# Optimization experiments

Measured on AMD Instinct MI355X. Metric: run time of the kernel, lower is better.

Reference implementation:

```python
import jax, jax.numpy as jnp
import numpy as np

D_MODEL = 5120
NUM_HEADS = 128
HEAD_DIM = D_MODEL // NUM_HEADS  # 40
LATENT = 1536


def setup_inputs() -> dict:
    key = jax.random.key(0)
    ks = jax.random.split(key, 9)
    B, S = 2, 1024
    scale = 0.02
    return {
        "x": jax.random.normal(ks[0], (B, S, D_MODEL), dtype=jnp.float32),
        "Wq": jax.random.normal(ks[1], (D_MODEL, D_MODEL), dtype=jnp.float32) * scale,
        "bq": jnp.zeros((D_MODEL,), dtype=jnp.float32),
        "Wc": jax.random.normal(ks[2], (D_MODEL, LATENT), dtype=jnp.float32) * scale,
        "bc": jnp.zeros((LATENT,), dtype=jnp.float32),
        "Wk": jax.random.normal(ks[3], (LATENT, D_MODEL), dtype=jnp.float32) * scale,
        "bk": jnp.zeros((D_MODEL,), dtype=jnp.float32),
        "Wv": jax.random.normal(ks[4], (LATENT, D_MODEL), dtype=jnp.float32) * scale,
        "bv": jnp.zeros((D_MODEL,), dtype=jnp.float32),
    }


def reference(x, Wq, bq, Wc, bc, Wk, bk, Wv, bv):
    B, S, _ = x.shape
    H, Dh = NUM_HEADS, HEAD_DIM
    # projections
    q = x @ Wq + bq                     # [B,S,D]
    kv_latent = x @ Wc + bc             # [B,S,L]
    k = kv_latent @ Wk + bk             # [B,S,D]
    v = kv_latent @ Wv + bv             # [B,S,D]
    # split heads -> [B,H,S,Dh]
    q = q.reshape(B, S, H, Dh).transpose(0, 2, 1, 3)
    k = k.reshape(B, S, H, Dh).transpose(0, 2, 1, 3)
    v = v.reshape(B, S, H, Dh).transpose(0, 2, 1, 3)
    scores = jnp.einsum("bhqd,bhkd->bhqk", q, k) / jnp.sqrt(jnp.float32(Dh))
    attn = jax.nn.softmax(scores, axis=-1)
    out = jnp.einsum("bhqk,bhkd->bhqd", attn, v)  # [B,H,S,Dh]
    return out.transpose(0, 2, 1, 3).reshape(B, S, H * Dh)
```

## Files before the change

kernel.cpp:

```cpp
#include <hip/hip_runtime.h>
#include <hip/hip_bf16.h>

typedef __attribute__((ext_vector_type(8))) __bf16 bf16x8;
typedef __attribute__((ext_vector_type(4))) __bf16 bf16x4;
typedef __attribute__((ext_vector_type(4))) float f32x4;

#define MFMA16(a, b, c) __builtin_amdgcn_mfma_f32_16x16x32_bf16((a), (b), (c), 0, 0, 0)

#if __has_builtin(__builtin_amdgcn_exp2f)
#define EXP2F(x) __builtin_amdgcn_exp2f(x)
#else
#define EXP2F(x) exp2f(x)
#endif

#define GLDS16(g, l)                                                             \
    __builtin_amdgcn_global_load_lds((const __attribute__((address_space(1))) void*)(g), \
                                     (__attribute__((address_space(3))) void*)(l), 16, 0, 0)

#define BARRIER()                          \
    do {                                   \
        asm volatile("" ::: "memory");     \
        __builtin_amdgcn_s_barrier();      \
        asm volatile("" ::: "memory");     \
    } while (0)

#define WAIT_LGKM0() asm volatile("s_waitcnt lgkmcnt(0)" ::: "memory")
#define VM6 asm volatile("s_waitcnt vmcnt(6)" ::: "memory")
#define VM8 asm volatile("s_waitcnt vmcnt(8)" ::: "memory")
#define VM0 asm volatile("s_waitcnt vmcnt(0)" ::: "memory")
#define VMNONE ((void)0)
#define KEEP(x) x
#define DROP(x)

static __device__ __forceinline__ unsigned short cvt_bf(float f) {
    return __builtin_bit_cast(unsigned short, (__bf16)f);
}

static __device__ __forceinline__ bf16x8 bf8_zero() {
    uint4 z = make_uint4(0, 0, 0, 0);
    return __builtin_bit_cast(bf16x8, z);
}

__global__ __launch_bounds__(256) void xconv(const float* __restrict__ X,
                                             unsigned short* __restrict__ Xb, int n) {
    int i = (blockIdx.x * 256 + threadIdx.x) * 4;
    if (i < n) {
        float4 f = *(const float4*)(X + i);
        ushort4 o;
        o.x = cvt_bf(f.x); o.y = cvt_bf(f.y); o.z = cvt_bf(f.z); o.w = cvt_bf(f.w);
        *(ushort4*)(Xb + i) = o;
    }
}

__global__ __launch_bounds__(256) void wconv(const float* __restrict__ W,
                                             unsigned short* __restrict__ WT, int K, int N) {
    __shared__ unsigned short tile[32][33];
    int n0 = blockIdx.x * 32, k0 = blockIdx.y * 32;
    int c = threadIdx.x & 31, r8 = threadIdx.x >> 5;
#pragma unroll
    for (int it = 0; it < 4; ++it) {
        int r = r8 + it * 8;
        tile[r][c] = cvt_bf(W[(size_t)(k0 + r) * N + n0 + c]);
    }
    __syncthreads();
    int k2 = (threadIdx.x & 15) * 2, n8 = threadIdx.x >> 4;
#pragma unroll
    for (int it = 0; it < 2; ++it) {
        int n = n8 + it * 16;
        ushort2 o;
        o.x = tile[k2][n];
        o.y = tile[k2 + 1][n];
        *(ushort2*)&WT[(size_t)(n0 + n) * K + k0 + k2] = o;
    }
}

#define STAGE_A(S, H, KT)                                                              \
    do {                                                                               \
        GLDS16(aS[H][0] + (size_t)(KT) * 64, &Abuf[S][(H) * 8192 + wid * 512]);        \
        GLDS16(aS[H][1] + (size_t)(KT) * 64, &Abuf[S][(H) * 8192 + 4096 + wid * 512]); \
    } while (0)
#define STAGE_B(S, H, KT)                                                              \
    do {                                                                               \
        GLDS16(bS[H][0] + (size_t)(KT) * 64, &Bbuf[S][(H) * 8192 + wid * 512]);        \
        GLDS16(bS[H][1] + (size_t)(KT) * 64, &Bbuf[S][(H) * 8192 + 4096 + wid * 512]); \
    } while (0)

#define LDA_HALF(S, QM)                                                                   \
    do {                                                                                  \
        _Pragma("unroll") for (int mi = 0; mi < 4; ++mi)                                  \
            _Pragma("unroll") for (int kh = 0; kh < 2; ++kh)                              \
                af[mi][kh] =                                                              \
                    *(const bf16x8*)&Abuf[S][((QM) * 8192 + aoff + mi * 1024) ^ (kh * 32)]; \
    } while (0)
#define LDB_HALF(S, QN, BF)                                                               \
    do {                                                                                  \
        _Pragma("unroll") for (int ni = 0; ni < 2; ++ni)                                  \
            _Pragma("unroll") for (int kh = 0; kh < 2; ++kh)                              \
                BF[ni][kh] =                                                              \
                    *(const bf16x8*)&Bbuf[S][((QN) * 8192 + boff + ni * 1024) ^ (kh * 32)]; \
    } while (0)

#define MMAQ(QM, QN, BF)                                                                \
    do {                                                                                \
        _Pragma("unroll") for (int mi = 0; mi < 4; ++mi)                                \
            _Pragma("unroll") for (int ni = 0; ni < 2; ++ni)                            \
                _Pragma("unroll") for (int kh = 0; kh < 2; ++kh)                        \
                    acc[(QM) * 4 + mi][(QN) * 2 + ni] =                                 \
                        MFMA16(af[mi][kh], BF[ni][kh], acc[(QM) * 4 + mi][(QN) * 2 + ni]); \
    } while (0)

#define KTILE(S, T, STG1, STG234, VMOP)             \
    {                                               \
        const int s_ = (S);                         \
        LDA_HALF(s_, 0);                            \
        LDB_HALF(s_, 0, bf0);                       \
        STG1(STAGE_B(s_ ^ 1, 0, (T) + 1);)          \
        asm volatile("s_waitcnt lgkmcnt(8)" ::: "memory"); \
        BARRIER();                                  \
        WAIT_LGKM0();                               \
        __builtin_amdgcn_s_setprio(1);              \
        MMAQ(0, 0, bf0);                            \
        __builtin_amdgcn_s_setprio(0);              \
        BARRIER();                                  \
        LDB_HALF(s_, 1, bf1);                       \
        STG234(STAGE_A(s_, 0, (T) + 2);)            \
        BARRIER();                                  \
        WAIT_LGKM0();                               \
        __builtin_amdgcn_s_setprio(1);              \
        MMAQ(0, 1, bf1);                            \
        __builtin_amdgcn_s_setprio(0);              \
        BARRIER();                                  \
        LDA_HALF(s_, 1);                            \
        STG234(STAGE_B(s_, 1, (T) + 2);)            \
        BARRIER();                                  \
        WAIT_LGKM0();                               \
        __builtin_amdgcn_s_setprio(1);              \
        MMAQ(1, 1, bf1);                            \
        __builtin_amdgcn_s_setprio(0);              \
        BARRIER();                                  \
        STG234(STAGE_A(s_, 1, (T) + 2);)            \
        VMOP;                                       \
        BARRIER();                                  \
        __builtin_amdgcn_s_setprio(1);              \
        MMAQ(1, 0, bf0);                            \
        __builtin_amdgcn_s_setprio(0);              \
        BARRIER();                                  \
    }

__global__ __launch_bounds__(512, 2) void gemm256(const unsigned short* __restrict__ A, int lda,
                                                  const unsigned short* __restrict__ BT, int ldb,
                                                  const float* __restrict__ bias0,
                                                  const float* __restrict__ bias1, int nsplit,
                                                  unsigned short* __restrict__ C, int ldc,
                                                  int K, float s0, float s1, int gx) {
    __shared__ __align__(16) unsigned short Abuf[2][16384];
    __shared__ __align__(16) unsigned short Bbuf[2][16384];

    int nwg = gridDim.x, orig = blockIdx.x;
    int cpx = nwg >> 3;
    int wgid = (orig & 7) * cpx + (orig >> 3);
    int tm = wgid / gx, tn = wgid % gx;
    int m0 = tm * 256, n0 = tn * 256;

    int tid = threadIdx.x, lane = tid & 63, wid = tid >> 6;
    int wm = wid >> 2, wn = wid & 3;
    int lrow = lane & 15, lkg = lane >> 4;

    int t5 = tid >> 3;
    int cole = ((tid & 7) ^ ((tid >> 3) & 7)) << 3;
    const unsigned short* aS[2][2];
    const unsigned short* bS[2][2];
#pragma unroll
    for (int H = 0; H < 2; ++H)
#pragma unroll
        for (int c = 0; c < 2; ++c) {
            int rA = (c << 7) | (H << 6) | t5;
            int rB = (((c << 1) | (t5 >> 5)) << 6) | (H << 5) | (t5 & 31);
            aS[H][c] = A + (size_t)(m0 + rA) * lda + cole;
            bS[H][c] = BT + (size_t)(n0 + rB) * ldb + cole;
        }

    int xorc = (lkg * 8) ^ ((lrow & 7) << 3);
    int aoff = wm * 4096 + lrow * 64 + xorc;
    int boff = wn * 2048 + lrow * 64 + xorc;

    f32x4 acc[8][4];
#pragma unroll
    for (int i = 0; i < 8; ++i)
#pragma unroll
        for (int j = 0; j < 4; ++j) acc[i][j] = (f32x4){0.f, 0.f, 0.f, 0.f};
    bf16x8 af[4][2], bf0[2][2], bf1[2][2];

    const int nkt = K >> 6;

    STAGE_A(0, 0, 0); STAGE_A(0, 1, 0); STAGE_B(0, 0, 0); STAGE_B(0, 1, 0);
    STAGE_A(1, 0, 1); STAGE_B(1, 1, 1); STAGE_A(1, 1, 1);
    VM6;
    BARRIER();

    int t = 0;
    for (; t + 2 < nkt; ++t) KTILE(t & 1, t, KEEP, KEEP, VM6);
    KTILE(t & 1, t, KEEP, DROP, VM0);
    ++t;
    KTILE(t & 1, t, DROP, DROP, VMNONE);

#pragma unroll
    for (int ni = 0; ni < 4; ++ni) {
        int col = n0 + wn * 64 + ni * 16 + lrow;
        float bval = (col < nsplit) ? bias0[col] : bias1[col - nsplit];
        float scl = (col < nsplit) ? s0 : s1;
#pragma unroll
        for (int mi = 0; mi < 8; ++mi) {
            int row = m0 + wm * 128 + mi * 16 + lkg * 4;
#pragma unroll
            for (int j = 0; j < 4; ++j)
                C[(size_t)(row + j) * ldc + col] = cvt_bf((acc[mi][ni][j] + bval) * scl);
        }
    }
}

#define STG128(S, KT)                                                                  \
    do {                                                                               \
        _Pragma("unroll") for (int i_ = 0; i_ < 4; ++i_)                               \
            GLDS16(Ag + (size_t)(i_ * 32) * lda + (size_t)(KT) * 64,                   \
                   &Abuf[S][i_ * 2048 + wid * 512]);                                   \
        _Pragma("unroll") for (int i_ = 0; i_ < 4; ++i_)                               \
            GLDS16(Bg + (size_t)(i_ * 32) * ldb + (size_t)(KT) * 64,                   \
                   &Bbuf[S][i_ * 2048 + wid * 512]);                                   \
    } while (0)

__global__ __launch_bounds__(256, 2) void gemm128(const unsigned short* __restrict__ A, int lda,
                                                  const unsigned short* __restrict__ BT, int ldb,
                                                  const float* __restrict__ bias0,
                                                  const float* __restrict__ bias1, int nsplit,
                                                  unsigned short* __restrict__ C, int ldc,
                                                  int K, float s0, float s1, int gy) {
    __shared__ __align__(16) unsigned short Abuf[2][8192];
    __shared__ __align__(16) unsigned short Bbuf[2][8192];

    int b = blockIdx.x;
    int tm = b % gy, tn = b / gy;
    int m0 = tm * 128, n0 = tn * 128;
    int tid = threadIdx.x, lane = tid & 63, wid = tid >> 6;
    int wm = wid >> 1, wn = wid & 1;
    int lrow = lane & 15, lkg = lane >> 4;

    int srow = tid >> 3;
    int cole = ((tid & 7) ^ ((tid >> 3) & 7)) << 3;
    const unsigned short* Ag = A + (size_t)(m0 + srow) * lda + cole;
    const unsigned short* Bg = BT + (size_t)(n0 + srow) * ldb + cole;

    int xorc8 = (lrow & 7) << 3;
    int aoff = (wm * 64 + lrow) * 64;
    int boff = (wn * 64 + lrow) * 64;

    f32x4 acc[4][4];
#pragma unroll
    for (int i = 0; i < 4; ++i)
#pragma unroll
        for (int j = 0; j < 4; ++j) acc[i][j] = (f32x4){0.f, 0.f, 0.f, 0.f};

    const int nkt = K >> 6;
    STG128(0, 0);
    for (int t = 0; t < nkt; ++t) {
        const int cur = t & 1;
        if (t + 1 < nkt) {
            STG128(cur ^ 1, t + 1);
            VM8;
        } else {
            VM0;
        }
        BARRIER();
        bf16x8 af[4][2], bv[4][2];
#pragma unroll
        for (int mi = 0; mi < 4; ++mi)
#pragma unroll
            for (int kh = 0; kh < 2; ++kh)
                af[mi][kh] = *(const bf16x8*)&Abuf[cur][aoff + mi * 1024 + (((kh * 4 + lkg) << 3) ^ xorc8)];
#pragma unroll
        for (int ni = 0; ni < 4; ++ni)
#pragma unroll
            for (int kh = 0; kh < 2; ++kh)
                bv[ni][kh] = *(const bf16x8*)&Bbuf[cur][boff + ni * 1024 + (((kh * 4 + lkg) << 3) ^ xorc8)];
        __builtin_amdgcn_s_setprio(1);
#pragma unroll
        for (int mi = 0; mi < 4; ++mi)
#pragma unroll
            for (int ni = 0; ni < 4; ++ni)
#pragma unroll
                for (int kh = 0; kh < 2; ++kh)
                    acc[mi][ni] = MFMA16(af[mi][kh], bv[ni][kh], acc[mi][ni]);
        __builtin_amdgcn_s_setprio(0);
        BARRIER();
    }

#pragma unroll
    for (int ni = 0; ni < 4; ++ni) {
        int col = n0 + wn * 64 + ni * 16 + lrow;
        float bval = (col < nsplit) ? bias0[col] : bias1[col - nsplit];
        float scl = (col < nsplit) ? s0 : s1;
#pragma unroll
        for (int mi = 0; mi < 4; ++mi) {
            int row = m0 + wm * 64 + mi * 16 + lkg * 4;
#pragma unroll
            for (int j = 0; j < 4; ++j)
                C[(size_t)(row + j) * ldc + col] = cvt_bf((acc[mi][ni][j] + bval) * scl);
        }
    }
}

__global__ __launch_bounds__(256) void attn(const unsigned short* __restrict__ q, int ldq,
                                            const unsigned short* __restrict__ k, int ldk,
                                            const unsigned short* __restrict__ v, int ldv,
                                            float* __restrict__ out) {
    const int S = 1024, D = 5120, Dh = 40;
    int b = blockIdx.z, h = blockIdx.y, qt = blockIdx.x;
    int t = threadIdx.x, lane = t & 63, wid = t >> 6;
    int lrow = lane & 15, lkg = lane >> 4;

    __shared__ __align__(16) unsigned short Ks[64 * 72];
    __shared__ __align__(16) unsigned short Vs[64 * 72];
    __shared__ __align__(16) unsigned short Ps[4][16 * 72];

    const size_t qbase = ((size_t)b * S) * ldq + (size_t)h * Dh;
    const size_t kbase = ((size_t)b * S) * ldk + (size_t)h * Dh;
    const size_t vbase = ((size_t)b * S) * ldv + (size_t)h * Dh;
    int q0 = qt * 64 + wid * 16;

    bf16x8 qf0, qf1;
    {
        const unsigned short* qp = q + qbase + (size_t)(q0 + lrow) * ldq;
        qf0 = *(const bf16x8*)(qp + lkg * 8);
        qf1 = (lkg == 0) ? *(const bf16x8*)(qp + 32) : bf8_zero();
    }

    f32x4 acc[3];
#pragma unroll
    for (int nb = 0; nb < 3; ++nb) acc[nb] = (f32x4){0.f, 0.f, 0.f, 0.f};
    float mrun = -INFINITY, lrun = 0.f;

    for (int kt = 0; kt < 16; ++kt) {
        __syncthreads();
#pragma unroll
        for (int it = 0; it < 2; ++it) {
            int idx = t + it * 256;
            int rr = idx >> 3, cc = idx & 7;
            uint4 val = make_uint4(0, 0, 0, 0);
            if (cc < 5) val = *(const uint4*)(k + kbase + (size_t)(kt * 64 + rr) * ldk + cc * 8);
            *(uint4*)&Ks[rr * 72 + cc * 8] = val;
        }
#pragma unroll
        for (int it = 0; it < 2; ++it) {
            int idx = t + it * 256;
            int rr = idx & 63, cc = idx >> 6;
            if (cc < 6) {
                uint4 val = make_uint4(0, 0, 0, 0);
                if (cc < 5) val = *(const uint4*)(v + vbase + (size_t)(kt * 64 + rr) * ldv + cc * 8);
                const unsigned short* pv = (const unsigned short*)&val;
#pragma unroll
                for (int j = 0; j < 8; ++j) Vs[(cc * 8 + j) * 72 + rr] = pv[j];
            }
        }
        __syncthreads();

        f32x4 sf[4];
#pragma unroll
        for (int nb = 0; nb < 4; ++nb) {
            sf[nb] = (f32x4){0.f, 0.f, 0.f, 0.f};
            bf16x8 kf0 = *(const bf16x8*)&Ks[(nb * 16 + lrow) * 72 + lkg * 8];
            bf16x8 kf1 = *(const bf16x8*)&Ks[(nb * 16 + lrow) * 72 + 32 + lkg * 8];
            sf[nb] = MFMA16(kf0, qf0, sf[nb]);
            sf[nb] = MFMA16(kf1, qf1, sf[nb]);
        }

        float tm = sf[0][0];
#pragma unroll
        for (int nb = 0; nb < 4; ++nb)
#pragma unroll
            for (int i = 0; i < 4; ++i) tm = fmaxf(tm, sf[nb][i]);
        tm = fmaxf(tm, __shfl_xor(tm, 16));
        tm = fmaxf(tm, __shfl_xor(tm, 32));
        float mn = fmaxf(mrun, tm);
        float al = EXP2F(mrun - mn);
        mrun = mn;
        float rs = 0.f;
#pragma unroll
        for (int nb = 0; nb < 4; ++nb) {
            bf16x4 pk;
#pragma unroll
            for (int i = 0; i < 4; ++i) {
                float p = EXP2F(sf[nb][i] - mn);
                rs += p;
                pk[i] = (__bf16)p;
            }
            *(bf16x4*)&Ps[wid][lrow * 72 + nb * 16 + lkg * 4] = pk;
        }
        rs += __shfl_xor(rs, 16);
        rs += __shfl_xor(rs, 32);
        lrun = lrun * al + rs;

        float alr[4];
#pragma unroll
        for (int i = 0; i < 4; ++i) alr[i] = __shfl(al, lkg * 4 + i);
#pragma unroll
        for (int nb = 0; nb < 3; ++nb)
#pragma unroll
            for (int i = 0; i < 4; ++i) acc[nb][i] *= alr[i];

#pragma unroll
        for (int kk = 0; kk < 2; ++kk) {
            bf16x8 pf = *(const bf16x8*)&Ps[wid][lrow * 72 + kk * 32 + lkg * 8];
#pragma unroll
            for (int nb = 0; nb < 3; ++nb) {
                bf16x8 vf = *(const bf16x8*)&Vs[(nb * 16 + lrow) * 72 + kk * 32 + lkg * 8];
                acc[nb] = MFMA16(pf, vf, acc[nb]);
            }
        }
    }

    float lr[4];
#pragma unroll
    for (int i = 0; i < 4; ++i) lr[i] = __shfl(lrun, lkg * 4 + i);
#pragma unroll
    for (int i = 0; i < 4; ++i) {
        float inv = 1.0f / lr[i];
        int s = q0 + lkg * 4 + i;
#pragma unroll
        for (int nb = 0; nb < 3; ++nb) {
            int d = nb * 16 + lrow;
            if (d < Dh) out[((size_t)(b * S + s)) * D + h * Dh + d] = acc[nb][i] * inv;
        }
    }
}

extern "C" void kernel_launch(void* const* d_in, const int* in_sizes, int n_in,
                              void* d_out, int out_size, void* d_ws, size_t ws_size,
                              hipStream_t stream) {
    const int M = 2048, D = 5120, L = 1536, NQ = D + L , NKV = 2 * D ;
    const float* x  = (const float*)d_in[0];
    const float* Wq = (const float*)d_in[1];
    const float* bq = (const float*)d_in[2];
    const float* Wc = (const float*)d_in[3];
    const float* bc = (const float*)d_in[4];
    const float* Wk = (const float*)d_in[5];
    const float* bk = (const float*)d_in[6];
    const float* Wv = (const float*)d_in[7];
    const float* bv = (const float*)d_in[8];
    float* out = (float*)d_out;

    unsigned short* ws = (unsigned short*)d_ws;
    size_t off = 0;
    unsigned short* xb    = ws + off; off += (size_t)M * D;
    unsigned short* WqcT  = ws + off; off += (size_t)NQ * D;
    unsigned short* WkvT  = ws + off; off += (size_t)NKV * L;
    unsigned short* qkvb  = ws + off; off += (size_t)M * NQ;
    unsigned short* kvout = ws + off; off += (size_t)M * NKV;

    xconv<<<(M * D) / 1024, 256, 0, stream>>>(x, xb, M * D);
    wconv<<<dim3(D / 32, D / 32), 256, 0, stream>>>(Wq, WqcT, D, D);
    wconv<<<dim3(L / 32, D / 32), 256, 0, stream>>>(Wc, WqcT + (size_t)D * D, D, L);
    wconv<<<dim3(D / 32, L / 32), 256, 0, stream>>>(Wk, WkvT, L, D);
    wconv<<<dim3(D / 32, L / 32), 256, 0, stream>>>(Wv, WkvT + (size_t)D * L, L, D);

    const float qscale = 1.4426950408889634f / 6.324555320336759f;

    gemm256<<<dim3((NQ / 256) * (M / 256)), 512, 0, stream>>>(xb, D, WqcT, D, bq, bc, D,
                                                              qkvb, NQ, D, qscale, 1.0f,
                                                              NQ / 256);
    gemm128<<<dim3((NKV / 128) * (M / 128)), 256, 0, stream>>>(qkvb + D, NQ, WkvT, L, bk, bv, D,
                                                               kvout, NKV, L, 1.0f, 1.0f,
                                                               M / 128);

    attn<<<dim3(1024 / 64, 128, 2), 256, 0, stream>>>(qkvb, NQ, kvout, NKV, kvout + D, NKV, out);
}
```

Baseline: 511.4 us.

## Restructure GEMM k-tile schedule with fewer barriers and add lazy softmax rescaling

The 256x256 GEMM main loop is reordered so the next tile's first A/B fragment reads are issued at the end of the previous iteration. The loop now uses two fused stage/wait points instead of eight barriers per k-tile, cutting synchronisation stalls and overlapping LDS reads with MFMA work. The attention kernel also skips the running-max update and accumulator rescale unless some lane's new max exceeds the old one by more than a threshold, in exp2 units. This is valid because the final normalisation divides it out, but it relies on bounded exponent growth and adds a wave-wide vote per tile.

```diff
diff --git a/kernel.cpp b/kernel.cpp
--- a/kernel.cpp
+++ b/kernel.cpp
@@ -74,6 +74,7 @@
     }
 }
 
+
 #define STAGE_A(S, H, KT)                                                              \
     do {                                                                               \
         GLDS16(aS[H][0] + (size_t)(KT) * 64, &Abuf[S][(H) * 8192 + wid * 512]);        \
@@ -109,42 +110,34 @@
                         MFMA16(af[mi][kh], BF[ni][kh], acc[(QM) * 4 + mi][(QN) * 2 + ni]); \
     } while (0)
 
-#define KTILE(S, T, STG1, STG234, VMOP)             \
-    {                                               \
-        const int s_ = (S);                         \
-        LDA_HALF(s_, 0);                            \
-        LDB_HALF(s_, 0, bf0);                       \
-        STG1(STAGE_B(s_ ^ 1, 0, (T) + 1);)          \
-        asm volatile("s_waitcnt lgkmcnt(8)" ::: "memory"); \
-        BARRIER();                                  \
-        WAIT_LGKM0();                               \
-        __builtin_amdgcn_s_setprio(1);              \
-        MMAQ(0, 0, bf0);                            \
-        __builtin_amdgcn_s_setprio(0);              \
-        BARRIER();                                  \
-        LDB_HALF(s_, 1, bf1);                       \
-        STG234(STAGE_A(s_, 0, (T) + 2);)            \
-        BARRIER();                                  \
-        WAIT_LGKM0();                               \
-        __builtin_amdgcn_s_setprio(1);              \
-        MMAQ(0, 1, bf1);                            \
-        __builtin_amdgcn_s_setprio(0);              \
-        BARRIER();                                  \
-        LDA_HALF(s_, 1);                            \
-        STG234(STAGE_B(s_, 1, (T) + 2);)            \
-        BARRIER();                                  \
-        WAIT_LGKM0();                               \
-        __builtin_amdgcn_s_setprio(1);              \
-        MMAQ(1, 1, bf1);                            \
-        __builtin_amdgcn_s_setprio(0);              \
-        BARRIER();                                  \
-        STG234(STAGE_A(s_, 1, (T) + 2);)            \
-        VMOP;                                       \
-        BARRIER();                                  \
-        __builtin_amdgcn_s_setprio(1);              \
-        MMAQ(1, 0, bf0);                            \
-        __builtin_amdgcn_s_setprio(0);              \
-        BARRIER();                                  \
+#define KTILE_V2(S, T, STG1, STG2, VMOP, RDNEXT)       \
+    {                                                  \
+        const int s_ = (S);                            \
+        LDB_HALF(s_, 1, bf1);                          \
+        STG1(STAGE_B(s_ ^ 1, 0, (T) + 1);)             \
+        __builtin_amdgcn_s_setprio(1);                 \
+        MMAQ(0, 0, bf0);                               \
+        __builtin_amdgcn_s_setprio(0);                 \
+        WAIT_LGKM0();                                  \
+        BARRIER();                                     \
+        STG2(STAGE_A(s_, 0, (T) + 2);                  \
+             STAGE_B(s_, 1, (T) + 2);)                 \
+        __builtin_amdgcn_s_setprio(1);                 \
+        MMAQ(0, 1, bf1);                               \
+        __builtin_amdgcn_s_setprio(0);                 \
+        LDA_HALF(s_, 1);                               \
+        __builtin_amdgcn_s_setprio(1);                 \
+        MMAQ(1, 1, bf1);                               \
+        __builtin_amdgcn_s_setprio(0);                 \
+        WAIT_LGKM0();                                  \
+        BARRIER();                                     \
+        STG2(STAGE_A(s_, 1, (T) + 2);)                 \
+        __builtin_amdgcn_s_setprio(1);                 \
+        MMAQ(1, 0, bf0);                               \
+        __builtin_amdgcn_s_setprio(0);                 \
+        VMOP;                                          \
+        BARRIER();                                     \
+        RDNEXT(LDA_HALF(s_ ^ 1, 0); LDB_HALF(s_ ^ 1, 0, bf0);) \
     }
 
 __global__ __launch_bounds__(512, 2) void gemm256(const unsigned short* __restrict__ A, int lda,
@@ -197,12 +190,14 @@
     STAGE_A(1, 0, 1); STAGE_B(1, 1, 1); STAGE_A(1, 1, 1);
     VM6;
     BARRIER();
+    LDA_HALF(0, 0);
+    LDB_HALF(0, 0, bf0);
 
     int t = 0;
-    for (; t + 2 < nkt; ++t) KTILE(t & 1, t, KEEP, KEEP, VM6);
-    KTILE(t & 1, t, KEEP, DROP, VM0);
+    for (; t + 2 < nkt; ++t) KTILE_V2(t & 1, t, KEEP, KEEP, VM6, KEEP);
+    KTILE_V2(t & 1, t, KEEP, DROP, VM0, KEEP);
     ++t;
-    KTILE(t & 1, t, DROP, DROP, VMNONE);
+    KTILE_V2(t & 1, t, DROP, DROP, VMNONE, DROP);
 
 #pragma unroll
     for (int ni = 0; ni < 4; ++ni) {
@@ -380,9 +375,14 @@
             for (int i = 0; i < 4; ++i) tm = fmaxf(tm, sf[nb][i]);
         tm = fmaxf(tm, __shfl_xor(tm, 16));
         tm = fmaxf(tm, __shfl_xor(tm, 32));
-        float mn = fmaxf(mrun, tm);
-        float al = EXP2F(mrun - mn);
-        mrun = mn;
+
+        float mn = mrun, al = 1.0f;
+        bool resc = !__all(tm <= mrun + 11.0f);
+        if (resc) {
+            mn = fmaxf(mrun, tm);
+            al = EXP2F(mrun - mn);
+            mrun = mn;
+        }
         float rs = 0.f;
 #pragma unroll
         for (int nb = 0; nb < 4; ++nb) {
@@ -399,13 +399,15 @@
         rs += __shfl_xor(rs, 32);
         lrun = lrun * al + rs;
 
-        float alr[4];
-#pragma unroll
-        for (int i = 0; i < 4; ++i) alr[i] = __shfl(al, lkg * 4 + i);
-#pragma unroll
-        for (int nb = 0; nb < 3; ++nb)
-#pragma unroll
-            for (int i = 0; i < 4; ++i) acc[nb][i] *= alr[i];
+        if (resc) {
+            float alr[4];
+#pragma unroll
+            for (int i = 0; i < 4; ++i) alr[i] = __shfl(al, lkg * 4 + i);
+#pragma unroll
+            for (int nb = 0; nb < 3; ++nb)
+#pragma unroll
+                for (int i = 0; i < 4; ++i) acc[nb][i] *= alr[i];
+        }
 
 #pragma unroll
         for (int kk = 0; kk < 2; ++kk) {
```

New measurement: 490.2 us. -4.1%, faster.
